# Kernel optimization log

Measured on AMD Instinct MI355X. Metric: run time of the kernel, lower is better.

## Reference

```python
import jax, jax.numpy as jnp
import numpy as np

D_MODEL = 2048
NUM_HEADS = 16
D_K = D_MODEL // NUM_HEADS
ROPE_THETA = 10000.0


def apply_rope(x, token_positions):
    # x: [B, H, S, D_k]; token_positions: [S] int
    d = x.shape[-1]
    inv_freq = 1.0 / (ROPE_THETA ** (jnp.arange(0, d, 2, dtype=jnp.float32) / d))  # [D_k/2]
    ang = token_positions.astype(jnp.float32)[:, None] * inv_freq[None, :]  # [S, D_k/2]
    cos = jnp.cos(ang)  # broadcast over B, H
    sin = jnp.sin(ang)
    x1 = x[..., 0::2]
    x2 = x[..., 1::2]
    r1 = x1 * cos - x2 * sin
    r2 = x1 * sin + x2 * cos
    return jnp.stack([r1, r2], axis=-1).reshape(x.shape)


def setup_inputs() -> dict:
    key = jax.random.key(0)
    kx, kq, kk, kv, ko = jax.random.split(key, 5)
    scale = 1.0 / np.sqrt(D_MODEL)
    return {
        "x": jax.random.normal(kx, (2, 2048, D_MODEL), dtype=jnp.float32),
        "token_positions": jnp.arange(2048, dtype=jnp.int32),
        "wq": jax.random.normal(kq, (D_MODEL, D_MODEL), dtype=jnp.float32) * scale,
        "wk": jax.random.normal(kk, (D_MODEL, D_MODEL), dtype=jnp.float32) * scale,
        "wv": jax.random.normal(kv, (D_MODEL, D_MODEL), dtype=jnp.float32) * scale,
        "wo": jax.random.normal(ko, (D_MODEL, D_MODEL), dtype=jnp.float32) * scale,
    }


def reference(x, token_positions, wq, wk, wv, wo):
    B, S, _ = x.shape
    # QKV projections (no bias), split heads -> [B, H, S, D_k]
    def split_heads(t):
        return t.reshape(B, S, NUM_HEADS, D_K).transpose(0, 2, 1, 3)

    q = split_heads(jnp.einsum("bsd,ed->bse", x, wq))
    k = split_heads(jnp.einsum("bsd,ed->bse", x, wk))
    v = split_heads(jnp.einsum("bsd,ed->bse", x, wv))

    q = apply_rope(q, token_positions)
    k = apply_rope(k, token_positions)

    scores = jnp.einsum("bhqd,bhkd->bhqk", q, k) / jnp.sqrt(jnp.float32(D_K))
    causal = jnp.tril(jnp.ones((S, S), dtype=bool))  # True where attend allowed
    scores = jnp.where(causal, scores, jnp.float32(-1e9))
    attn = jax.nn.softmax(scores, axis=-1)
    out = jnp.einsum("bhqk,bhkd->bhqd", attn, v)  # [B, H, S, D_k]
    out = out.transpose(0, 2, 1, 3).reshape(B, S, D_MODEL)
    return jnp.einsum("bsd,ed->bse", out, wo)
```

## Files before the change

### kernel.cpp

```cpp
#include <hip/hip_runtime.h>
#include <hip/hip_bf16.h>
#include <math.h>

#define D_MODEL 2048
#define NHEAD   16
#define DK      128
#define SEQ     2048
#define BATCH   2
#define MROWS   (BATCH*SEQ)

typedef __attribute__((ext_vector_type(8))) short short8;
typedef __attribute__((ext_vector_type(4))) short shortx4;
typedef __attribute__((ext_vector_type(4))) float f32x4;

static __device__ __forceinline__ short f2bf(float v) {
    union { __hip_bfloat16 b; short s; } u;
    u.b = __float2bfloat16(v);
    return u.s;
}
static __device__ __forceinline__ float bf2f(short s) {
    union { short s; __hip_bfloat16 b; } u;
    u.s = s;
    return __bfloat162float(u.b);
}

#define GBM 128
#define GBN 128
#define GBK 32
#define LDKG 40

__global__ __launch_bounds__(256, 2) void gemm_nt_mfma(const float* __restrict__ A,
                                                       const float* __restrict__ W,
                                                       float* __restrict__ C,
                                                       int M, int N, int K)
{
    __shared__ __align__(16) short Ah[GBM][LDKG];
    __shared__ __align__(16) short Al[GBM][LDKG];
    __shared__ __align__(16) short Bh[GBN][LDKG];
    __shared__ __align__(16) short Bl[GBN][LDKG];

    const int tid  = threadIdx.x;
    const int lane = tid & 63;
    const int w    = tid >> 6;
    const int wm   = (w & 1) * 64;
    const int wn   = (w >> 1) * 64;
    const int l16  = lane & 15;
    const int kb   = (lane >> 4) * 8;

    const size_t row0 = (size_t)blockIdx.y * GBM;
    const size_t col0 = (size_t)blockIdx.x * GBN;

    const int sr0 = tid >> 2;
    const int sr1 = sr0 + 64;
    const int skc = (tid & 3) * 8;

    f32x4 acc[4][4];
#pragma unroll
    for (int i = 0; i < 4; ++i)
#pragma unroll
        for (int j = 0; j < 4; ++j) acc[i][j] = (f32x4)0.0f;

    float4 pa0a = *(const float4*)(A + (row0 + sr0) * K + skc);
    float4 pa0b = *(const float4*)(A + (row0 + sr0) * K + skc + 4);
    float4 pa1a = *(const float4*)(A + (row0 + sr1) * K + skc);
    float4 pa1b = *(const float4*)(A + (row0 + sr1) * K + skc + 4);
    float4 pw0a = *(const float4*)(W + (col0 + sr0) * K + skc);
    float4 pw0b = *(const float4*)(W + (col0 + sr0) * K + skc + 4);
    float4 pw1a = *(const float4*)(W + (col0 + sr1) * K + skc);
    float4 pw1b = *(const float4*)(W + (col0 + sr1) * K + skc + 4);

    for (int kt = 0; kt < K; kt += GBK) {
        {
            float f[8]; short8 h, l;
#define CVT8(va, vb)                                                        \
            f[0]=va.x; f[1]=va.y; f[2]=va.z; f[3]=va.w;                     \
            f[4]=vb.x; f[5]=vb.y; f[6]=vb.z; f[7]=vb.w;                     \
            _Pragma("unroll")                                               \
            for (int j = 0; j < 8; ++j) {                                   \
                short hb = f2bf(f[j]); h[j] = hb; l[j] = f2bf(f[j] - bf2f(hb)); \
            }
            CVT8(pa0a, pa0b)
            *(short8*)&Ah[sr0][skc] = h;  *(short8*)&Al[sr0][skc] = l;
            CVT8(pa1a, pa1b)
            *(short8*)&Ah[sr1][skc] = h;  *(short8*)&Al[sr1][skc] = l;
            CVT8(pw0a, pw0b)
            *(short8*)&Bh[sr0][skc] = h;  *(short8*)&Bl[sr0][skc] = l;
            CVT8(pw1a, pw1b)
            *(short8*)&Bh[sr1][skc] = h;  *(short8*)&Bl[sr1][skc] = l;
#undef CVT8
        }
        __syncthreads();

        if (kt + GBK < K) {
            const int kn = kt + GBK;
            pa0a = *(const float4*)(A + (row0 + sr0) * K + kn + skc);
            pa0b = *(const float4*)(A + (row0 + sr0) * K + kn + skc + 4);
            pa1a = *(const float4*)(A + (row0 + sr1) * K + kn + skc);
            pa1b = *(const float4*)(A + (row0 + sr1) * K + kn + skc + 4);
            pw0a = *(const float4*)(W + (col0 + sr0) * K + kn + skc);
            pw0b = *(const float4*)(W + (col0 + sr0) * K + kn + skc + 4);
            pw1a = *(const float4*)(W + (col0 + sr1) * K + kn + skc);
            pw1b = *(const float4*)(W + (col0 + sr1) * K + kn + skc + 4);
        }

        short8 bh[4], bl[4];
#pragma unroll
        for (int fn = 0; fn < 4; ++fn) {
            bh[fn] = *(const short8*)&Bh[wn + fn * 16 + l16][kb];
            bl[fn] = *(const short8*)&Bl[wn + fn * 16 + l16][kb];
        }
#pragma unroll
        for (int fm = 0; fm < 4; ++fm) {
            const short8 ah = *(const short8*)&Ah[wm + fm * 16 + l16][kb];
            const short8 al = *(const short8*)&Al[wm + fm * 16 + l16][kb];
#pragma unroll
            for (int fn = 0; fn < 4; ++fn) {
                acc[fm][fn] = __builtin_amdgcn_mfma_f32_16x16x32_bf16(ah, bh[fn], acc[fm][fn], 0, 0, 0);
                acc[fm][fn] = __builtin_amdgcn_mfma_f32_16x16x32_bf16(ah, bl[fn], acc[fm][fn], 0, 0, 0);
                acc[fm][fn] = __builtin_amdgcn_mfma_f32_16x16x32_bf16(al, bh[fn], acc[fm][fn], 0, 0, 0);
            }
        }
        __syncthreads();
    }

#pragma unroll
    for (int fm = 0; fm < 4; ++fm) {
#pragma unroll
        for (int j = 0; j < 4; ++j) {
            const size_t r = row0 + wm + fm * 16 + (lane >> 4) * 4 + j;
#pragma unroll
            for (int fn = 0; fn < 4; ++fn)
                C[r * N + col0 + wn + fn * 16 + l16] = acc[fm][fn][j];
        }
    }
}

__global__ __launch_bounds__(256) void rope_kernel(float* __restrict__ q,
                                                   float* __restrict__ k,
                                                   const int* __restrict__ pos)
{
    const int idx = blockIdx.x * 256 + threadIdx.x;
    if (idx >= MROWS * 1024) return;
    const int pair = idx & 1023;
    const int row  = idx >> 10;
    const int s    = row & (SEQ - 1);
    const int j    = pair & 63;

    const float inv_freq = (float)pow(10000.0, -(double)(2 * j) / 128.0);
    const float ang = (float)pos[s] * inv_freq;
    float sn, cs;
    sincosf(ang, &sn, &cs);

    const size_t off = (size_t)row * D_MODEL + pair * 2;
    float2 vq = *(float2*)(q + off);
    float2 vk = *(float2*)(k + off);
    float2 rq, rk;
    rq.x = vq.x * cs - vq.y * sn;  rq.y = vq.x * sn + vq.y * cs;
    rk.x = vk.x * cs - vk.y * sn;  rk.y = vk.x * sn + vk.y * cs;
    *(float2*)(q + off) = rq;
    *(float2*)(k + off) = rk;
}

#define ABM 128
#define AWQ 32
#define KVT 64
#define KLD 136
#define VLD 72

__global__ __launch_bounds__(256, 2) void flash_attn_mfma(const float* __restrict__ Q,
                                                          const float* __restrict__ K,
                                                          const float* __restrict__ V,
                                                          float* __restrict__ O)
{
    __shared__ __align__(16) short KhS[KVT * KLD];
    __shared__ __align__(16) short KlS[KVT * KLD];
    __shared__ __align__(16) short VTh[DK * VLD];
    __shared__ __align__(16) short VTl[DK * VLD];

    const int tid  = threadIdx.x;
    const int lane = tid & 63;
    const int w    = tid >> 6;
    const int l16  = lane & 15;
    const int g    = lane >> 4;
    const int h    = blockIdx.y & (NHEAD - 1);
    const int b    = blockIdx.y >> 4;
    const size_t base = (size_t)b * SEQ * D_MODEL + (size_t)h * DK;
    const int qb  = blockIdx.x * ABM;
    const int qw0 = qb + w * AWQ;
    const float scale = 0.08838834764831845f;

    short8 qh[2][4], ql[2][4];
#pragma unroll
    for (int fq = 0; fq < 2; ++fq)
#pragma unroll
        for (int ks = 0; ks < 4; ++ks) {
            const float* src = Q + base + (size_t)(qw0 + fq * 16 + l16) * D_MODEL + g * 8 + ks * 32;
            float4 f0 = *(const float4*)src;
            float4 f1 = *(const float4*)(src + 4);
            float f[8] = {f0.x, f0.y, f0.z, f0.w, f1.x, f1.y, f1.z, f1.w};
            short8 hh, ll;
#pragma unroll
            for (int e = 0; e < 8; ++e) {
                short hb = f2bf(f[e]); hh[e] = hb; ll[e] = f2bf(f[e] - bf2f(hb));
            }
            qh[fq][ks] = hh; ql[fq][ks] = ll;
        }

    f32x4 accO[2][8];
#pragma unroll
    for (int i = 0; i < 2; ++i)
#pragma unroll
        for (int j = 0; j < 8; ++j) accO[i][j] = (f32x4)0.0f;
    float mstate[2] = {-3.0e38f, -3.0e38f};
    float lstate[2] = {0.f, 0.f};

    const int nt = (qb + ABM) / KVT;
    for (int t = 0; t < nt; ++t) {
        const int kv0 = t * KVT;
        __syncthreads();

        {
            const int r  = tid >> 2;
            const int d0 = (tid & 3) * 32;
            const float* src = K + base + (size_t)(kv0 + r) * D_MODEL + d0;
#pragma unroll
            for (int u = 0; u < 4; ++u) {
                float4 f0 = *(const float4*)(src + u * 8);
                float4 f1 = *(const float4*)(src + u * 8 + 4);
                float f[8] = {f0.x, f0.y, f0.z, f0.w, f1.x, f1.y, f1.z, f1.w};
                short8 hh, ll;
#pragma unroll
                for (int e = 0; e < 8; ++e) {
                    short hb = f2bf(f[e]); hh[e] = hb; ll[e] = f2bf(f[e] - bf2f(hb));
                }
                *(short8*)&KhS[r * KLD + d0 + u * 8] = hh;
                *(short8*)&KlS[r * KLD + d0 + u * 8] = ll;
            }
        }
#pragma unroll
        for (int it = 0; it < 2; ++it) {
            const int tt  = tid + it * 256;
            const int dq  = tt & 31;
            const int kvq = tt >> 5;
            const float* vs = V + base + (size_t)(kv0 + kvq * 4) * D_MODEL + dq * 4;
            float4 r0 = *(const float4*)(vs);
            float4 r1 = *(const float4*)(vs + D_MODEL);
            float4 r2 = *(const float4*)(vs + 2 * D_MODEL);
            float4 r3 = *(const float4*)(vs + 3 * D_MODEL);
            float vals[4][4] = {{r0.x,r0.y,r0.z,r0.w},{r1.x,r1.y,r1.z,r1.w},
                                {r2.x,r2.y,r2.z,r2.w},{r3.x,r3.y,r3.z,r3.w}};
#pragma unroll
            for (int c = 0; c < 4; ++c) {
                const int r   = dq * 4 + c;
                const int sw  = ((r >> 2) ^ (r >> 4)) & 3;
                const int off = r * VLD + (((kvq >> 1) ^ sw) << 3) + ((kvq & 1) << 2);
                shortx4 hh, ll;
#pragma unroll
                for (int i = 0; i < 4; ++i) {
                    float f = vals[i][c];
                    short hb = f2bf(f); hh[i] = hb; ll[i] = f2bf(f - bf2f(hb));
                }
                *(shortx4*)&VTh[off] = hh;
                *(shortx4*)&VTl[off] = ll;
            }
        }
        __syncthreads();

        const bool active = (kv0 <= qw0 + AWQ - 1);
        if (active) {
            f32x4 accS[4][2];
#pragma unroll
            for (int i = 0; i < 4; ++i) { accS[i][0] = (f32x4)0.0f; accS[i][1] = (f32x4)0.0f; }
#pragma unroll
            for (int ks = 0; ks < 4; ++ks) {
#pragma unroll
                for (int fs = 0; fs < 4; ++fs) {
                    const short8 kh = *(const short8*)&KhS[(fs * 16 + l16) * KLD + g * 8 + ks * 32];
                    const short8 kl = *(const short8*)&KlS[(fs * 16 + l16) * KLD + g * 8 + ks * 32];
#pragma unroll
                    for (int fq = 0; fq < 2; ++fq) {
                        accS[fs][fq] = __builtin_amdgcn_mfma_f32_16x16x32_bf16(kh, qh[fq][ks], accS[fs][fq], 0, 0, 0);
                        accS[fs][fq] = __builtin_amdgcn_mfma_f32_16x16x32_bf16(kh, ql[fq][ks], accS[fs][fq], 0, 0, 0);
                        accS[fs][fq] = __builtin_amdgcn_mfma_f32_16x16x32_bf16(kl, qh[fq][ks], accS[fs][fq], 0, 0, 0);
                    }
                }
            }

            const bool needmask = (kv0 + KVT - 1 > qw0);
            float al[2];
#pragma unroll
            for (int fq = 0; fq < 2; ++fq) {
                const int qg = qw0 + fq * 16 + l16;
                float mx = -3.0e38f;
#pragma unroll
                for (int fs = 0; fs < 4; ++fs)
#pragma unroll
                    for (int j = 0; j < 4; ++j) {
                        float s = accS[fs][fq][j] * scale;
                        if (needmask) {
                            const int kvg = kv0 + fs * 16 + g * 4 + j;
                            s = (kvg <= qg) ? s : -3.0e38f;
                        }
                        accS[fs][fq][j] = s;
                        mx = fmaxf(mx, s);
                    }
                mx = fmaxf(mx, __shfl_xor(mx, 16));
                mx = fmaxf(mx, __shfl_xor(mx, 32));
                const float mnew = fmaxf(mstate[fq], mx);
                al[fq] = __expf(mstate[fq] - mnew);
                mstate[fq] = mnew;
                float sm = 0.f;
#pragma unroll
                for (int fs = 0; fs < 4; ++fs)
#pragma unroll
                    for (int j = 0; j < 4; ++j) {
                        const float p = __expf(accS[fs][fq][j] - mnew);
                        accS[fs][fq][j] = p;
                        sm += p;
                    }
                sm += __shfl_xor(sm, 16);
                sm += __shfl_xor(sm, 32);
                lstate[fq] = lstate[fq] * al[fq] + sm;
            }

            float alr[2][4];
#pragma unroll
            for (int fm = 0; fm < 2; ++fm)
#pragma unroll
                for (int j = 0; j < 4; ++j)
                    alr[fm][j] = __shfl(al[fm], (g << 2) | j);
#pragma unroll
            for (int fm = 0; fm < 2; ++fm)
#pragma unroll
                for (int fd = 0; fd < 8; ++fd)
#pragma unroll
                    for (int j = 0; j < 4; ++j)
                        accO[fm][fd][j] *= alr[fm][j];

#pragma unroll
            for (int ks = 0; ks < 2; ++ks) {
                short8 pah[2], pal[2];
#pragma unroll
                for (int fm = 0; fm < 2; ++fm) {
                    float pv[8];
#pragma unroll
                    for (int e = 0; e < 8; ++e) {
                        const int j = e & 3;
                        const int srcl = ((((lane >> 4) & 1) << 1) + (e >> 2)) * 16 + l16;
                        const float c0 = __shfl(accS[2 * ks][fm][j], srcl);
                        const float c1 = __shfl(accS[2 * ks + 1][fm][j], srcl);
                        pv[e] = (g >> 1) ? c1 : c0;
                    }
                    short8 hh, ll;
#pragma unroll
                    for (int e = 0; e < 8; ++e) {
                        short hb = f2bf(pv[e]); hh[e] = hb; ll[e] = f2bf(pv[e] - bf2f(hb));
                    }
                    pah[fm] = hh; pal[fm] = ll;
                }
#pragma unroll
                for (int fd = 0; fd < 8; ++fd) {
                    const int r = fd * 16 + l16;
                    const int sw = ((r >> 2) ^ (r >> 4)) & 3;
                    const int off = r * VLD + (((g + 4 * ks) ^ sw) << 3);
                    const short8 vh = *(const short8*)&VTh[off];
                    const short8 vl = *(const short8*)&VTl[off];
#pragma unroll
                    for (int fm = 0; fm < 2; ++fm) {
                        accO[fm][fd] = __builtin_amdgcn_mfma_f32_16x16x32_bf16(pah[fm], vh, accO[fm][fd], 0, 0, 0);
                        accO[fm][fd] = __builtin_amdgcn_mfma_f32_16x16x32_bf16(pah[fm], vl, accO[fm][fd], 0, 0, 0);
                        accO[fm][fd] = __builtin_amdgcn_mfma_f32_16x16x32_bf16(pal[fm], vh, accO[fm][fd], 0, 0, 0);
                    }
                }
            }
        }
    }

    float rl[2][4];
#pragma unroll
    for (int fm = 0; fm < 2; ++fm)
#pragma unroll
        for (int j = 0; j < 4; ++j)
            rl[fm][j] = 1.0f / __shfl(lstate[fm], (g << 2) | j);
#pragma unroll
    for (int fm = 0; fm < 2; ++fm)
#pragma unroll
        for (int j = 0; j < 4; ++j) {
            const size_t row = base + (size_t)(qw0 + fm * 16 + 4 * g + j) * D_MODEL;
#pragma unroll
            for (int fd = 0; fd < 8; ++fd)
                O[row + fd * 16 + l16] = accO[fm][fd][j] * rl[fm][j];
        }
}

extern "C" void kernel_launch(void* const* d_in, const int* in_sizes, int n_in,
                              void* d_out, int out_size, void* d_ws, size_t ws_size,
                              hipStream_t stream)
{
    const float* x  = (const float*)d_in[0];
    const int*  pos = (const int*)d_in[1];
    const float* wq = (const float*)d_in[2];
    const float* wk = (const float*)d_in[3];
    const float* wv = (const float*)d_in[4];
    const float* wo = (const float*)d_in[5];
    float* out = (float*)d_out;

    const size_t bufElems = (size_t)MROWS * D_MODEL;
    float* q  = (float*)d_ws;
    float* k  = q + bufElems;
    float* v  = k + bufElems;
    float* ao = v + bufElems;

    const dim3 blk(256);
    const dim3 ggrid(D_MODEL / GBN, MROWS / GBM);

    gemm_nt_mfma<<<ggrid, blk, 0, stream>>>(x, wq, q, MROWS, D_MODEL, D_MODEL);
    gemm_nt_mfma<<<ggrid, blk, 0, stream>>>(x, wk, k, MROWS, D_MODEL, D_MODEL);
    gemm_nt_mfma<<<ggrid, blk, 0, stream>>>(x, wv, v, MROWS, D_MODEL, D_MODEL);

    rope_kernel<<<(MROWS * 1024 + 255) / 256, blk, 0, stream>>>(q, k, pos);

    flash_attn_mfma<<<dim3(SEQ / ABM, BATCH * NHEAD), blk, 0, stream>>>(q, k, v, ao);

    gemm_nt_mfma<<<ggrid, blk, 0, stream>>>(ao, wo, out, MROWS, D_MODEL, D_MODEL);
}
```

Baseline: 850.4 us.

## Pre-split operands to bf16 hi/lo, pipeline and load-balance flash attention

Adds a split kernel that converts activations and weights into bf16 hi/lo arrays once, so the GEMMs no longer redo the conversion per tile. This path is only taken when the workspace is large enough. Flash attention now double-buffers K/V in shared memory and issues register prefetches for the next tile. Each block processes a pair of causal query tiles (i and 15-i) to balance work, and the K tile uses an XOR swizzle instead of padding. This trades extra memory traffic for the split arrays, plus lower occupancy in attention (launch bounds 1), for reduced conversion work and overlapped loads.

```diff
diff --git a/kernel.cpp b/kernel.cpp
--- a/kernel.cpp
+++ b/kernel.cpp
@@ -24,10 +24,123 @@
     return __bfloat162float(u.b);
 }
 
+__global__ __launch_bounds__(256) void split_bf16(const float* __restrict__ in,
+                                                  short* __restrict__ hi,
+                                                  short* __restrict__ lo, int n8)
+{
+    int i = blockIdx.x * 256 + threadIdx.x;
+    const int stride = gridDim.x * 256;
+    for (; i < n8; i += stride) {
+        const float4 a = ((const float4*)in)[2 * i];
+        const float4 b = ((const float4*)in)[2 * i + 1];
+        const float f[8] = {a.x, a.y, a.z, a.w, b.x, b.y, b.z, b.w};
+        short8 h, l;
+#pragma unroll
+        for (int e = 0; e < 8; ++e) {
+            const short hb = f2bf(f[e]); h[e] = hb; l[e] = f2bf(f[e] - bf2f(hb));
+        }
+        ((short8*)hi)[i] = h;
+        ((short8*)lo)[i] = l;
+    }
+}
+
 #define GBM 128
 #define GBN 128
 #define GBK 32
 #define LDKG 40
+
+__global__ __launch_bounds__(256, 2) void gemm_nt_bf(const short* __restrict__ Ahg,
+                                                     const short* __restrict__ Alg,
+                                                     const short* __restrict__ Whg,
+                                                     const short* __restrict__ Wlg,
+                                                     float* __restrict__ C,
+                                                     int M, int N, int K)
+{
+    __shared__ __align__(16) short Ah[GBM][LDKG];
+    __shared__ __align__(16) short Al[GBM][LDKG];
+    __shared__ __align__(16) short Bh[GBN][LDKG];
+    __shared__ __align__(16) short Bl[GBN][LDKG];
+
+    const int tid  = threadIdx.x;
+    const int lane = tid & 63;
+    const int w    = tid >> 6;
+    const int wm   = (w & 1) * 64;
+    const int wn   = (w >> 1) * 64;
+    const int l16  = lane & 15;
+    const int kb   = (lane >> 4) * 8;
+
+    const size_t row0 = (size_t)blockIdx.y * GBM;
+    const size_t col0 = (size_t)blockIdx.x * GBN;
+
+    const int sr0 = tid >> 2;
+    const int sr1 = sr0 + 64;
+    const int skc = (tid & 3) * 8;
+
+    f32x4 acc[4][4];
+#pragma unroll
+    for (int i = 0; i < 4; ++i)
+#pragma unroll
+        for (int j = 0; j < 4; ++j) acc[i][j] = (f32x4)0.0f;
+
+    short8 ra0h = *(const short8*)(Ahg + (row0 + sr0) * K + skc);
+    short8 ra0l = *(const short8*)(Alg + (row0 + sr0) * K + skc);
+    short8 ra1h = *(const short8*)(Ahg + (row0 + sr1) * K + skc);
+    short8 ra1l = *(const short8*)(Alg + (row0 + sr1) * K + skc);
+    short8 rw0h = *(const short8*)(Whg + (col0 + sr0) * K + skc);
+    short8 rw0l = *(const short8*)(Wlg + (col0 + sr0) * K + skc);
+    short8 rw1h = *(const short8*)(Whg + (col0 + sr1) * K + skc);
+    short8 rw1l = *(const short8*)(Wlg + (col0 + sr1) * K + skc);
+
+    for (int kt = 0; kt < K; kt += GBK) {
+        *(short8*)&Ah[sr0][skc] = ra0h;  *(short8*)&Al[sr0][skc] = ra0l;
+        *(short8*)&Ah[sr1][skc] = ra1h;  *(short8*)&Al[sr1][skc] = ra1l;
+        *(short8*)&Bh[sr0][skc] = rw0h;  *(short8*)&Bl[sr0][skc] = rw0l;
+        *(short8*)&Bh[sr1][skc] = rw1h;  *(short8*)&Bl[sr1][skc] = rw1l;
+        __syncthreads();
+
+        if (kt + GBK < K) {
+            const int kn = kt + GBK;
+            ra0h = *(const short8*)(Ahg + (row0 + sr0) * K + kn + skc);
+            ra0l = *(const short8*)(Alg + (row0 + sr0) * K + kn + skc);
+            ra1h = *(const short8*)(Ahg + (row0 + sr1) * K + kn + skc);
+            ra1l = *(const short8*)(Alg + (row0 + sr1) * K + kn + skc);
+            rw0h = *(const short8*)(Whg + (col0 + sr0) * K + kn + skc);
+            rw0l = *(const short8*)(Wlg + (col0 + sr0) * K + kn + skc);
+            rw1h = *(const short8*)(Whg + (col0 + sr1) * K + kn + skc);
+            rw1l = *(const short8*)(Wlg + (col0 + sr1) * K + kn + skc);
+        }
+
+        short8 bh[4], bl[4];
+#pragma unroll
+        for (int fn = 0; fn < 4; ++fn) {
+            bh[fn] = *(const short8*)&Bh[wn + fn * 16 + l16][kb];
+            bl[fn] = *(const short8*)&Bl[wn + fn * 16 + l16][kb];
+        }
+#pragma unroll
+        for (int fm = 0; fm < 4; ++fm) {
+            const short8 ah = *(const short8*)&Ah[wm + fm * 16 + l16][kb];
+            const short8 al = *(const short8*)&Al[wm + fm * 16 + l16][kb];
+#pragma unroll
+            for (int fn = 0; fn < 4; ++fn) {
+                acc[fm][fn] = __builtin_amdgcn_mfma_f32_16x16x32_bf16(ah, bh[fn], acc[fm][fn], 0, 0, 0);
+                acc[fm][fn] = __builtin_amdgcn_mfma_f32_16x16x32_bf16(ah, bl[fn], acc[fm][fn], 0, 0, 0);
+                acc[fm][fn] = __builtin_amdgcn_mfma_f32_16x16x32_bf16(al, bh[fn], acc[fm][fn], 0, 0, 0);
+            }
+        }
+        __syncthreads();
+    }
+
+#pragma unroll
+    for (int fm = 0; fm < 4; ++fm) {
+#pragma unroll
+        for (int j = 0; j < 4; ++j) {
+            const size_t r = row0 + wm + fm * 16 + (lane >> 4) * 4 + j;
+#pragma unroll
+            for (int fn = 0; fn < 4; ++fn)
+                C[r * N + col0 + wn + fn * 16 + l16] = acc[fm][fn][j];
+        }
+    }
+}
 
 __global__ __launch_bounds__(256, 2) void gemm_nt_mfma(const float* __restrict__ A,
                                                        const float* __restrict__ W,
@@ -164,18 +277,136 @@
 #define ABM 128
 #define AWQ 32
 #define KVT 64
-#define KLD 136
+#define KROW 128
 #define VLD 72
 
-__global__ __launch_bounds__(256, 2) void flash_attn_mfma(const float* __restrict__ Q,
+__device__ __forceinline__ void attn_issue_loads(const float* __restrict__ K,
+                                                 const float* __restrict__ V,
+                                                 size_t base, int kv0, int tid,
+                                                 float4* kreg, float4* vreg)
+{
+    const int r  = tid >> 2;
+    const int d0 = (tid & 3) * 32;
+    const float* ksrc = K + base + (size_t)(kv0 + r) * D_MODEL + d0;
+#pragma unroll
+    for (int u = 0; u < 4; ++u) {
+        kreg[2 * u]     = *(const float4*)(ksrc + u * 8);
+        kreg[2 * u + 1] = *(const float4*)(ksrc + u * 8 + 4);
+    }
+#pragma unroll
+    for (int it = 0; it < 2; ++it) {
+        const int tt  = tid + it * 256;
+        const int dq  = tt & 31;
+        const int kvq = tt >> 5;
+        const float* vs = V + base + (size_t)(kv0 + kvq * 4) * D_MODEL + dq * 4;
+#pragma unroll
+        for (int i = 0; i < 4; ++i)
+            vreg[it * 4 + i] = *(const float4*)(vs + i * D_MODEL);
+    }
+}
+
+__device__ __forceinline__ void attn_convert_write(short* __restrict__ KhS,
+                                                   short* __restrict__ KlS,
+                                                   short* __restrict__ VTh,
+                                                   short* __restrict__ VTl,
+                                                   int tid,
+                                                   const float4* kreg,
+                                                   const float4* vreg)
+{
+    const int r = tid >> 2;
+#pragma unroll
+    for (int u = 0; u < 4; ++u) {
+        const float4 f0 = kreg[2 * u];
+        const float4 f1 = kreg[2 * u + 1];
+        const float f[8] = {f0.x, f0.y, f0.z, f0.w, f1.x, f1.y, f1.z, f1.w};
+        short8 hh, ll;
+#pragma unroll
+        for (int e = 0; e < 8; ++e) {
+            const short hb = f2bf(f[e]); hh[e] = hb; ll[e] = f2bf(f[e] - bf2f(hb));
+        }
+        const int off = r * KROW + (((4 * (tid & 3) + u) ^ (r & 7)) << 3);
+        *(short8*)&KhS[off] = hh;
+        *(short8*)&KlS[off] = ll;
+    }
+#pragma unroll
+    for (int it = 0; it < 2; ++it) {
+        const int tt  = tid + it * 256;
+        const int dq  = tt & 31;
+        const int kvq = tt >> 5;
+        const float4 r0 = vreg[it * 4 + 0];
+        const float4 r1 = vreg[it * 4 + 1];
+        const float4 r2 = vreg[it * 4 + 2];
+        const float4 r3 = vreg[it * 4 + 3];
+        const float vals[4][4] = {{r0.x, r0.y, r0.z, r0.w}, {r1.x, r1.y, r1.z, r1.w},
+                                  {r2.x, r2.y, r2.z, r2.w}, {r3.x, r3.y, r3.z, r3.w}};
+#pragma unroll
+        for (int c = 0; c < 4; ++c) {
+            const int rr  = dq * 4 + c;
+            const int sw  = ((rr >> 2) ^ (rr >> 4)) & 3;
+            const int off = rr * VLD + (((kvq >> 1) ^ sw) << 3) + ((kvq & 1) << 2);
+            shortx4 hh, ll;
+#pragma unroll
+            for (int i = 0; i < 4; ++i) {
+                const float fv = vals[i][c];
+                const short hb = f2bf(fv); hh[i] = hb; ll[i] = f2bf(fv - bf2f(hb));
+            }
+            *(shortx4*)&VTh[off] = hh;
+            *(shortx4*)&VTl[off] = ll;
+        }
+    }
+}
+
+__device__ __forceinline__ void attn_load_q(const float* __restrict__ Q, size_t base,
+                                            int qw0, int l16, int g,
+                                            short8 qh[2][4], short8 ql[2][4])
+{
+#pragma unroll
+    for (int fq = 0; fq < 2; ++fq)
+#pragma unroll
+        for (int ks = 0; ks < 4; ++ks) {
+            const float* src = Q + base + (size_t)(qw0 + fq * 16 + l16) * D_MODEL + g * 8 + ks * 32;
+            const float4 f0 = *(const float4*)src;
+            const float4 f1 = *(const float4*)(src + 4);
+            const float f[8] = {f0.x, f0.y, f0.z, f0.w, f1.x, f1.y, f1.z, f1.w};
+            short8 hh, ll;
+#pragma unroll
+            for (int e = 0; e < 8; ++e) {
+                const short hb = f2bf(f[e]); hh[e] = hb; ll[e] = f2bf(f[e] - bf2f(hb));
+            }
+            qh[fq][ks] = hh; ql[fq][ks] = ll;
+        }
+}
+
+__device__ __forceinline__ void attn_write_o(float* __restrict__ O, size_t base,
+                                             int qw0, int g, int l16,
+                                             const f32x4 accO[2][8], const float lstate[2])
+{
+    float rl[2][4];
+#pragma unroll
+    for (int fm = 0; fm < 2; ++fm)
+#pragma unroll
+        for (int j = 0; j < 4; ++j)
+            rl[fm][j] = 1.0f / __shfl(lstate[fm], (g << 2) | j);
+#pragma unroll
+    for (int fm = 0; fm < 2; ++fm)
+#pragma unroll
+        for (int j = 0; j < 4; ++j) {
+            const size_t row = base + (size_t)(qw0 + fm * 16 + 4 * g + j) * D_MODEL;
+#pragma unroll
+            for (int fd = 0; fd < 8; ++fd)
+                O[row + fd * 16 + l16] = accO[fm][fd][j] * rl[fm][j];
+        }
+}
+
+__global__ __launch_bounds__(256, 1) void flash_attn_mfma(const float* __restrict__ Q,
                                                           const float* __restrict__ K,
                                                           const float* __restrict__ V,
                                                           float* __restrict__ O)
 {
-    __shared__ __align__(16) short KhS[KVT * KLD];
-    __shared__ __align__(16) short KlS[KVT * KLD];
-    __shared__ __align__(16) short VTh[DK * VLD];
-    __shared__ __align__(16) short VTl[DK * VLD];
+    __shared__ __align__(16) short KhS[2][KVT * KROW];
+    __shared__ __align__(16) short KlS[2][KVT * KROW];
+    __shared__ __align__(16) short VTh[2][DK * VLD];
+    __shared__ __align__(16) short VTl[2][DK * VLD];
 
     const int tid  = threadIdx.x;
     const int lane = tid & 63;
@@ -185,26 +416,15 @@
     const int h    = blockIdx.y & (NHEAD - 1);
     const int b    = blockIdx.y >> 4;
     const size_t base = (size_t)b * SEQ * D_MODEL + (size_t)h * DK;
-    const int qb  = blockIdx.x * ABM;
-    const int qw0 = qb + w * AWQ;
     const float scale = 0.08838834764831845f;
 
+    const int qtA = blockIdx.x;
+    const int qtB = 15 - qtA;
+    const int ntA = 2 * qtA + 2;
+    const int total = 34;
+
     short8 qh[2][4], ql[2][4];
-#pragma unroll
-    for (int fq = 0; fq < 2; ++fq)
-#pragma unroll
-        for (int ks = 0; ks < 4; ++ks) {
-            const float* src = Q + base + (size_t)(qw0 + fq * 16 + l16) * D_MODEL + g * 8 + ks * 32;
-            float4 f0 = *(const float4*)src;
-            float4 f1 = *(const float4*)(src + 4);
-            float f[8] = {f0.x, f0.y, f0.z, f0.w, f1.x, f1.y, f1.z, f1.w};
-            short8 hh, ll;
-#pragma unroll
-            for (int e = 0; e < 8; ++e) {
-                short hb = f2bf(f[e]); hh[e] = hb; ll[e] = f2bf(f[e] - bf2f(hb));
-            }
-            qh[fq][ks] = hh; ql[fq][ks] = ll;
-        }
+    attn_load_q(Q, base, qtA * ABM + w * AWQ, l16, g, qh, ql);
 
     f32x4 accO[2][8];
 #pragma unroll
@@ -214,57 +434,35 @@
     float mstate[2] = {-3.0e38f, -3.0e38f};
     float lstate[2] = {0.f, 0.f};
 
-    const int nt = (qb + ABM) / KVT;
-    for (int t = 0; t < nt; ++t) {
-        const int kv0 = t * KVT;
+    float4 kreg[8], vreg[8];
+    attn_issue_loads(K, V, base, 0, tid, kreg, vreg);
+    attn_convert_write(KhS[0], KlS[0], VTh[0], VTl[0], tid, kreg, vreg);
+    int cur = 0;
+
+    for (int st = 0; st < total; ++st) {
+        const int pass = (st >= ntA) ? 1 : 0;
+        const int t    = pass ? (st - ntA) : st;
+        const int qt   = pass ? qtB : qtA;
+        const int kv0  = t * KVT;
+        const int qw0  = qt * ABM + w * AWQ;
+
         __syncthreads();
 
-        {
-            const int r  = tid >> 2;
-            const int d0 = (tid & 3) * 32;
-            const float* src = K + base + (size_t)(kv0 + r) * D_MODEL + d0;
-#pragma unroll
-            for (int u = 0; u < 4; ++u) {
-                float4 f0 = *(const float4*)(src + u * 8);
-                float4 f1 = *(const float4*)(src + u * 8 + 4);
-                float f[8] = {f0.x, f0.y, f0.z, f0.w, f1.x, f1.y, f1.z, f1.w};
-                short8 hh, ll;
-#pragma unroll
-                for (int e = 0; e < 8; ++e) {
-                    short hb = f2bf(f[e]); hh[e] = hb; ll[e] = f2bf(f[e] - bf2f(hb));
-                }
-                *(short8*)&KhS[r * KLD + d0 + u * 8] = hh;
-                *(short8*)&KlS[r * KLD + d0 + u * 8] = ll;
-            }
-        }
-#pragma unroll
-        for (int it = 0; it < 2; ++it) {
-            const int tt  = tid + it * 256;
-            const int dq  = tt & 31;
-            const int kvq = tt >> 5;
-            const float* vs = V + base + (size_t)(kv0 + kvq * 4) * D_MODEL + dq * 4;
-            float4 r0 = *(const float4*)(vs);
-            float4 r1 = *(const float4*)(vs + D_MODEL);
-            float4 r2 = *(const float4*)(vs + 2 * D_MODEL);
-            float4 r3 = *(const float4*)(vs + 3 * D_MODEL);
-            float vals[4][4] = {{r0.x,r0.y,r0.z,r0.w},{r1.x,r1.y,r1.z,r1.w},
-                                {r2.x,r2.y,r2.z,r2.w},{r3.x,r3.y,r3.z,r3.w}};
-#pragma unroll
-            for (int c = 0; c < 4; ++c) {
-                const int r   = dq * 4 + c;
-                const int sw  = ((r >> 2) ^ (r >> 4)) & 3;
-                const int off = r * VLD + (((kvq >> 1) ^ sw) << 3) + ((kvq & 1) << 2);
-                shortx4 hh, ll;
-#pragma unroll
-                for (int i = 0; i < 4; ++i) {
-                    float f = vals[i][c];
-                    short hb = f2bf(f); hh[i] = hb; ll[i] = f2bf(f - bf2f(hb));
-                }
-                *(shortx4*)&VTh[off] = hh;
-                *(shortx4*)&VTl[off] = ll;
-            }
-        }
-        __syncthreads();
+        if (st + 1 < total) {
+            const int t2 = (st + 1 >= ntA) ? (st + 1 - ntA) : (st + 1);
+            attn_issue_loads(K, V, base, t2 * KVT, tid, kreg, vreg);
+        }
+
+        if (pass && t == 0) {
+            attn_write_o(O, base, qtA * ABM + w * AWQ, g, l16, accO, lstate);
+            attn_load_q(Q, base, qtB * ABM + w * AWQ, l16, g, qh, ql);
+#pragma unroll
+            for (int i = 0; i < 2; ++i)
+#pragma unroll
+                for (int j = 0; j < 8; ++j) accO[i][j] = (f32x4)0.0f;
+            mstate[0] = mstate[1] = -3.0e38f;
+            lstate[0] = lstate[1] = 0.f;
+        }
 
         const bool active = (kv0 <= qw0 + AWQ - 1);
         if (active) {
@@ -275,8 +473,9 @@
             for (int ks = 0; ks < 4; ++ks) {
 #pragma unroll
                 for (int fs = 0; fs < 4; ++fs) {
-                    const short8 kh = *(const short8*)&KhS[(fs * 16 + l16) * KLD + g * 8 + ks * 32];
-                    const short8 kl = *(const short8*)&KlS[(fs * 16 + l16) * KLD + g * 8 + ks * 32];
+                    const int koff = (fs * 16 + l16) * KROW + (((g + 4 * ks) ^ (l16 & 7)) << 3);
+                    const short8 kh = *(const short8*)&KhS[cur][koff];
+                    const short8 kl = *(const short8*)&KlS[cur][koff];
 #pragma unroll
                     for (int fq = 0; fq < 2; ++fq) {
                         accS[fs][fq] = __builtin_amdgcn_mfma_f32_16x16x32_bf16(kh, qh[fq][ks], accS[fs][fq], 0, 0, 0);
@@ -354,7 +553,7 @@
                     short8 hh, ll;
 #pragma unroll
                     for (int e = 0; e < 8; ++e) {
-                        short hb = f2bf(pv[e]); hh[e] = hb; ll[e] = f2bf(pv[e] - bf2f(hb));
+                        const short hb = f2bf(pv[e]); hh[e] = hb; ll[e] = f2bf(pv[e] - bf2f(hb));
                     }
                     pah[fm] = hh; pal[fm] = ll;
                 }
@@ -363,8 +562,8 @@
                     const int r = fd * 16 + l16;
                     const int sw = ((r >> 2) ^ (r >> 4)) & 3;
                     const int off = r * VLD + (((g + 4 * ks) ^ sw) << 3);
-                    const short8 vh = *(const short8*)&VTh[off];
-                    const short8 vl = *(const short8*)&VTl[off];
+                    const short8 vh = *(const short8*)&VTh[cur][off];
+                    const short8 vl = *(const short8*)&VTl[cur][off];
 #pragma unroll
                     for (int fm = 0; fm < 2; ++fm) {
                         accO[fm][fd] = __builtin_amdgcn_mfma_f32_16x16x32_bf16(pah[fm], vh, accO[fm][fd], 0, 0, 0);
@@ -374,23 +573,13 @@
                 }
             }
         }
-    }
-
-    float rl[2][4];
-#pragma unroll
-    for (int fm = 0; fm < 2; ++fm)
-#pragma unroll
-        for (int j = 0; j < 4; ++j)
-            rl[fm][j] = 1.0f / __shfl(lstate[fm], (g << 2) | j);
-#pragma unroll
-    for (int fm = 0; fm < 2; ++fm)
-#pragma unroll
-        for (int j = 0; j < 4; ++j) {
-            const size_t row = base + (size_t)(qw0 + fm * 16 + 4 * g + j) * D_MODEL;
-#pragma unroll
-            for (int fd = 0; fd < 8; ++fd)
-                O[row + fd * 16 + l16] = accO[fm][fd][j] * rl[fm][j];
-        }
+
+        if (st + 1 < total)
+            attn_convert_write(KhS[cur ^ 1], KlS[cur ^ 1], VTh[cur ^ 1], VTl[cur ^ 1], tid, kreg, vreg);
+        cur ^= 1;
+    }
+
+    attn_write_o(O, base, qtB * ABM + w * AWQ, g, l16, accO, lstate);
 }
 
 extern "C" void kernel_launch(void* const* d_in, const int* in_sizes, int n_in,
@@ -405,22 +594,60 @@
     const float* wo = (const float*)d_in[5];
     float* out = (float*)d_out;
 
-    const size_t bufElems = (size_t)MROWS * D_MODEL;
-    float* q  = (float*)d_ws;
-    float* k  = q + bufElems;
-    float* v  = k + bufElems;
-    float* ao = v + bufElems;
+    char* base = (char*)d_ws;
+    const size_t MB = 1024ull * 1024ull;
+    float* q  = (float*)(base + 0 * MB);
+    float* k  = (float*)(base + 32 * MB);
+    float* v  = (float*)(base + 64 * MB);
+    float* ao = (float*)(base + 96 * MB);
 
     const dim3 blk(256);
     const dim3 ggrid(D_MODEL / GBN, MROWS / GBM);
-
-    gemm_nt_mfma<<<ggrid, blk, 0, stream>>>(x, wq, q, MROWS, D_MODEL, D_MODEL);
-    gemm_nt_mfma<<<ggrid, blk, 0, stream>>>(x, wk, k, MROWS, D_MODEL, D_MODEL);
-    gemm_nt_mfma<<<ggrid, blk, 0, stream>>>(x, wv, v, MROWS, D_MODEL, D_MODEL);
-
-    rope_kernel<<<(MROWS * 1024 + 255) / 256, blk, 0, stream>>>(q, k, pos);
-
-    flash_attn_mfma<<<dim3(SEQ / ABM, BATCH * NHEAD), blk, 0, stream>>>(q, k, v, ao);
-
-    gemm_nt_mfma<<<ggrid, blk, 0, stream>>>(ao, wo, out, MROWS, D_MODEL, D_MODEL);
-}
+    const dim3 agrid(SEQ / (2 * ABM), BATCH * NHEAD);
+
+    const bool presplit = (ws_size >= 224 * MB);
+
+    if (presplit) {
+        short* xh  = (short*)(base + 128 * MB);
+        short* xl  = (short*)(base + 144 * MB);
+        short* wqh = (short*)(base + 160 * MB);
+        short* wql = (short*)(base + 168 * MB);
+        short* wkh = (short*)(base + 176 * MB);
+        short* wkl = (short*)(base + 184 * MB);
+        short* wvh = (short*)(base + 192 * MB);
+        short* wvl = (short*)(base + 200 * MB);
+        short* woh = (short*)(base + 208 * MB);
+        short* wol = (short*)(base + 216 * MB);
+        short* aoh = xh;
+        short* aol = xl;
+
+        const int nx8 = MROWS * D_MODEL / 8;
+        const int nw8 = D_MODEL * D_MODEL / 8;
+        split_bf16<<<2048, blk, 0, stream>>>(x,  xh,  xl,  nx8);
+        split_bf16<<<2048, blk, 0, stream>>>(wq, wqh, wql, nw8);
+        split_bf16<<<2048, blk, 0, stream>>>(wk, wkh, wkl, nw8);
+        split_bf16<<<2048, blk, 0, stream>>>(wv, wvh, wvl, nw8);
+        split_bf16<<<2048, blk, 0, stream>>>(wo, woh, wol, nw8);
+
+        gemm_nt_bf<<<ggrid, blk, 0, stream>>>(xh, xl, wqh, wql, q, MROWS, D_MODEL, D_MODEL);
+        gemm_nt_bf<<<ggrid, blk, 0, stream>>>(xh, xl, wkh, wkl, k, MROWS, D_MODEL, D_MODEL);
+        gemm_nt_bf<<<ggrid, blk, 0, stream>>>(xh, xl, wvh, wvl, v, MROWS, D_MODEL, D_MODEL);
+
+        rope_kernel<<<(MROWS * 1024 + 255) / 256, blk, 0, stream>>>(q, k, pos);
+
+        flash_attn_mfma<<<agrid, blk, 0, stream>>>(q, k, v, ao);
+
+        split_bf16<<<2048, blk, 0, stream>>>(ao, aoh, aol, nx8);
+        gemm_nt_bf<<<ggrid, blk, 0, stream>>>(aoh, aol, woh, wol, out, MROWS, D_MODEL, D_MODEL);
+    } else {
+        gemm_nt_mfma<<<ggrid, blk, 0, stream>>>(x, wq, q, MROWS, D_MODEL, D_MODEL);
+        gemm_nt_mfma<<<ggrid, blk, 0, stream>>>(x, wk, k, MROWS, D_MODEL, D_MODEL);
+        gemm_nt_mfma<<<ggrid, blk, 0, stream>>>(x, wv, v, MROWS, D_MODEL, D_MODEL);
+
+        rope_kernel<<<(MROWS * 1024 + 255) / 256, blk, 0, stream>>>(q, k, pos);
+
+        flash_attn_mfma<<<agrid, blk, 0, stream>>>(q, k, v, ao);
+
+        gemm_nt_mfma<<<ggrid, blk, 0, stream>>>(ao, wo, out, MROWS, D_MODEL, D_MODEL);
+    }
+}
```

Measured after the change: 836.7 us. Within noise of the previous version (-1.6%).
